# Kernel tuning notes

Measured on AMD Instinct MI355X. Metric: run time of the kernel, lower is better.

## Reference

```python
import jax, jax.numpy as jnp
import numpy as np

ALPHA = 0.2  # leaky_relu negative slope
NFEAT = 3    # node_feat_size for final tanh slice


def _init_linear(key, out_f, in_f):
    kw, kb = jax.random.split(key)
    scale = 1.0 / np.sqrt(in_f)
    w = jax.random.uniform(kw, (out_f, in_f), jnp.float32, -scale, scale)
    b = jax.random.uniform(kb, (out_f,), jnp.float32, -scale, scale)
    return w, b


def setup_inputs() -> dict:
    key = jax.random.key(0)
    ks = jax.random.split(key, 8)
    B, N, H = 64, 100, 32
    inp = {"x": jax.random.normal(ks[0], (B, N, H), jnp.float32)}
    # fe: [65 -> 96 -> 160 -> 192]; fn: [224 -> 256 -> 256 -> 32]
    fe_dims = [(96, 65), (160, 96), (192, 160)]
    fn_dims = [(256, 224), (256, 256), (32, 256)]
    for i, (o, f) in enumerate(fe_dims):
        w, b = _init_linear(ks[1 + i], o, f)
        inp[f"fe_w{i}"] = w
        inp[f"fe_b{i}"] = b
    for i, (o, f) in enumerate(fn_dims):
        w, b = _init_linear(ks[4 + i], o, f)
        inp[f"fn_w{i}"] = w
        inp[f"fn_b{i}"] = b
    return inp


def _forward(x, fe_params, fn_params):
    B, N, H = x.shape
    # --- getA: all-pairs edge features (pos_diffs) ---
    x1 = jnp.broadcast_to(x[:, :, None, :], (B, N, N, H))  # sender i
    x2 = jnp.broadcast_to(x[:, None, :, :], (B, N, N, H))  # receiver j
    dists = jnp.linalg.norm(x2[..., :2] - x1[..., :2] + 1e-12, axis=-1, keepdims=True)
    A = jnp.concatenate([x1, x2, dists], axis=-1)  # [B,N,N,2H+1]
    # --- edge MLP (all layers with leaky_relu) ---
    for w, b in fe_params:
        A = jax.nn.leaky_relu(jnp.einsum("bijf,of->bijo", A, w) + b, ALPHA)
    # sum-aggregate over neighbor axis j
    A = jnp.sum(A, axis=2)  # [B,N,fe_out]
    # --- node MLP (leaky_relu on all but last) ---
    h = jnp.concatenate([A, x], axis=-1)  # [B,N,fe_out+H]
    for w, b in fn_params[:-1]:
        h = jax.nn.leaky_relu(jnp.einsum("bnf,of->bno", h, w) + b, ALPHA)
    w, b = fn_params[-1]
    h = jnp.einsum("bnf,of->bno", h, w) + b  # [B,N,H]
    return jnp.tanh(h[..., :NFEAT])


def reference(x, fe_w0, fe_b0, fe_w1, fe_b1, fe_w2, fe_b2,
              fn_w0, fn_b0, fn_w1, fn_b1, fn_w2, fn_b2):
    fe_params = [(fe_w0, fe_b0), (fe_w1, fe_b1), (fe_w2, fe_b2)]
    fn_params = [(fn_w0, fn_b0), (fn_w1, fn_b1), (fn_w2, fn_b2)]
    return _forward(x, fe_params, fn_params)
```

## Files before the change

kernel.cpp:

```cpp
#include <hip/hip_runtime.h>
#include <math.h>

#define ALPHA 0.2f

typedef __attribute__((ext_vector_type(8))) short bf16x8;
typedef __attribute__((ext_vector_type(4))) float f32x4;

static __device__ __forceinline__ float lrelu(float v) {
    return fmaxf(v, ALPHA * v);
}
static __device__ __forceinline__ uint16_t f2b(float f) {
    union { float f; uint32_t u; } c; c.f = f;
    const uint32_t u = c.u + 0x7FFFu + ((c.u >> 16) & 1u);
    return (uint16_t)(u >> 16);
}
static __device__ __forceinline__ uint32_t cvt2(float lo, float hi) {
    uint32_t r;
    asm("v_cvt_pk_bf16_f32 %0, %1, %2" : "=v"(r) : "v"(lo), "v"(hi));
    return r;
}

__global__ __launch_bounds__(256) void precompute(
    const float* __restrict__ x, const float* __restrict__ w0,
    const float* __restrict__ b0, const float* __restrict__ w1,
    const float* __restrict__ w2, const float* __restrict__ f0,
    const float* __restrict__ f1,
    float* __restrict__ base0T, float* __restrict__ Gp,
    float* __restrict__ xyt, float* __restrict__ wd0,
    uint16_t* __restrict__ wb1, uint16_t* __restrict__ wb2,
    uint16_t* __restrict__ wfn0, uint16_t* __restrict__ wfn1,
    float* __restrict__ hin)
{
    const int blk = blockIdx.x, t = threadIdx.x;
    if (blk >= 256) {
        const int t0 = (blk - 256) * 256 + t;
        for (int i = t0; i < 160 * 96;  i += 7168) wb1[i]  = f2b(w1[i]);
        for (int i = t0; i < 192 * 160; i += 7168) wb2[i]  = f2b(w2[i]);
        for (int i = t0; i < 256 * 224; i += 7168) wfn0[i] = f2b(f0[i]);
        for (int i = t0; i < 256 * 256; i += 7168) wfn1[i] = f2b(f1[i]);
        if (t0 < 96) wd0[t0] = w0[t0 * 65 + 64];
        return;
    }
    __shared__ float W0s[96 * 65];
    __shared__ float xs[25 * 32];
    const int r0 = blk * 25;
    for (int i = t; i < 96 * 65; i += 256) W0s[i] = w0[i];
    for (int i = t; i < 800; i += 256) xs[i] = x[r0 * 32 + i];
    __syncthreads();
    for (int it = 0; it < 19; ++it) {
        const int q = t + 256 * it;
        if (q < 4800) {
            const int row = q / 192, oi = q - row * 192;
            const int o = (oi < 96) ? oi : oi - 96;
            const float* wr = W0s + o * 65 + ((oi < 96) ? 0 : 32);
            const float* xr = xs + row * 32;
            float a = (oi < 96) ? b0[o] : 0.0f;
#pragma unroll
            for (int k = 0; k < 32; ++k) a += wr[k] * xr[k];
            if (oi < 96) base0T[(r0 + row) * 96 + o] = a;
            else         Gp[(o >> 3) * 51200 + (r0 + row) * 8 + (o & 7)] = a;
        }
    }
    for (int i = t; i < 50; i += 256)
        xyt[(r0 + (i >> 1)) * 2 + (i & 1)] = xs[(i >> 1) * 32 + (i & 1)];
    for (int i = t; i < 800; i += 256)
        hin[(r0 + (i >> 5)) * 256 + 192 + (i & 31)] = xs[i];
}

__global__ __launch_bounds__(256, 3) void edge_kernel(
    const float* __restrict__ base0T, const float* __restrict__ Gp,
    const float* __restrict__ xyt, const float* __restrict__ wd0,
    const float* __restrict__ b1f, const float* __restrict__ b2f,
    const uint16_t* __restrict__ wb1, const uint16_t* __restrict__ wb2,
    float* __restrict__ hin, float* __restrict__ PB)
{
    __shared__ __align__(16) uint16_t H1[64 * 104];
    __shared__ __align__(16) uint16_t H2[64 * 168];

    const int bi = blockIdx.x >> 1, half = blockIdx.x & 1, b = bi / 100;
    const int t = threadIdx.x, lane = t & 63, w = t >> 6;
    const int col = lane & 15, g = lane >> 4;
    const int MT = half ? 3 : 4;

    const float2 pi = *(const float2*)(xyt + 2 * bi);

    for (int q = t; q < 768; q += 256) {
        const int row = q & 63, c8 = q >> 6;
        const int jloc = half * 64 + row;
        uint16_t* dst = H1 + row * 104 + c8 * 8;
        if (jloc < 100) {
            const int jg = b * 100 + jloc;
            const float2 pj = *(const float2*)(xyt + 2 * jg);
            const float dx = pj.x - pi.x + 1e-12f, dy = pj.y - pi.y + 1e-12f;
            const float d = sqrtf(dx * dx + dy * dy);
            const int ow = c8 * 8;
            const float* gp = Gp + c8 * 51200 + jg * 8;
            const f32x4 g0 = *(const f32x4*)(gp);
            const f32x4 g1 = *(const f32x4*)(gp + 4);
            const f32x4 c0 = *(const f32x4*)(base0T + bi * 96 + ow);
            const f32x4 c1 = *(const f32x4*)(base0T + bi * 96 + ow + 4);
            const f32x4 w0v = *(const f32x4*)(wd0 + ow);
            const f32x4 w1v = *(const f32x4*)(wd0 + ow + 4);
            float v[8];
#pragma unroll
            for (int e = 0; e < 4; ++e) {
                v[e]     = lrelu(g0[e] + c0[e] + w0v[e] * d);
                v[4 + e] = lrelu(g1[e] + c1[e] + w1v[e] * d);
            }
            *(uint4*)dst = (uint4){cvt2(v[0], v[1]), cvt2(v[2], v[3]),
                                   cvt2(v[4], v[5]), cvt2(v[6], v[7])};
        } else {
            *(uint4*)dst = (uint4){0u, 0u, 0u, 0u};
        }
    }
    __syncthreads();

    {
        f32x4 acc[3][4];
#pragma unroll
        for (int s = 0; s < 3; ++s) {
            const int nt = w + 4 * s;
            if (nt < 10) {
#pragma unroll
                for (int m = 0; m < 4; ++m) if (m < MT) {
                    float bv = b1f[nt * 16 + col];
                    if (half && m == 2 && g != 0) bv = 0.0f;
                    acc[s][m] = (f32x4){bv, bv, bv, bv};
                }
            }
        }
        __builtin_amdgcn_s_setprio(1);
#pragma unroll
        for (int kt = 0; kt < 3; ++kt) {
            bf16x8 bfr[3];
#pragma unroll
            for (int s = 0; s < 3; ++s) {
                const int nt = w + 4 * s;
                if (nt < 10)
                    bfr[s] = *(const bf16x8*)(wb1 + (nt * 16 + col) * 96 + kt * 32 + 8 * g);
            }
#pragma unroll
            for (int m = 0; m < 4; ++m) if (m < MT) {
                const bf16x8 af = *(const bf16x8*)(H1 + (m * 16 + col) * 104 + kt * 32 + 8 * g);
#pragma unroll
                for (int s = 0; s < 3; ++s) {
                    const int nt = w + 4 * s;
                    if (nt < 10)
                        acc[s][m] = __builtin_amdgcn_mfma_f32_16x16x32_bf16(af, bfr[s], acc[s][m], 0, 0, 0);
                }
            }
        }
        __builtin_amdgcn_s_setprio(0);
#pragma unroll
        for (int s = 0; s < 3; ++s) {
            const int nt = w + 4 * s;
            if (nt < 10) {
#pragma unroll
                for (int m = 0; m < 4; ++m) if (m < MT) {
                    const uint32_t p01 = cvt2(lrelu(acc[s][m][0]), lrelu(acc[s][m][1]));
                    const uint32_t p23 = cvt2(lrelu(acc[s][m][2]), lrelu(acc[s][m][3]));
                    const int base = (m * 16 + 4 * g) * 168 + nt * 16 + col;
                    H2[base]       = (uint16_t)p01;
                    H2[base + 168] = (uint16_t)(p01 >> 16);
                    H2[base + 336] = (uint16_t)p23;
                    H2[base + 504] = (uint16_t)(p23 >> 16);
                }
            }
        }
    }
    __syncthreads();

    {
        f32x4 acc[3][4];
#pragma unroll
        for (int s = 0; s < 3; ++s) {
            const int nt = w + 4 * s;
#pragma unroll
            for (int m = 0; m < 4; ++m) if (m < MT) {
                float bv = b2f[nt * 16 + col];
                if (half && m == 2 && g != 0) bv = 0.0f;
                acc[s][m] = (f32x4){bv, bv, bv, bv};
            }
        }
        __builtin_amdgcn_s_setprio(1);
#pragma unroll
        for (int kt = 0; kt < 5; ++kt) {
            bf16x8 bfr[3];
#pragma unroll
            for (int s = 0; s < 3; ++s) {
                const int nt = w + 4 * s;
                bfr[s] = *(const bf16x8*)(wb2 + (nt * 16 + col) * 160 + kt * 32 + 8 * g);
            }
#pragma unroll
            for (int m = 0; m < 4; ++m) if (m < MT) {
                const bf16x8 af = *(const bf16x8*)(H2 + (m * 16 + col) * 168 + kt * 32 + 8 * g);
#pragma unroll
                for (int s = 0; s < 3; ++s)
                    acc[s][m] = __builtin_amdgcn_mfma_f32_16x16x32_bf16(af, bfr[s], acc[s][m], 0, 0, 0);
            }
        }
        __builtin_amdgcn_s_setprio(0);
        float* dst = half ? (PB + bi * 192) : (hin + bi * 256);
#pragma unroll
        for (int s = 0; s < 3; ++s) {
            float ps = 0.0f;
#pragma unroll
            for (int m = 0; m < 4; ++m) if (m < MT) {
#pragma unroll
                for (int r = 0; r < 4; ++r)
                    ps += lrelu(acc[s][m][r]);
            }
            ps += __shfl_xor(ps, 16);
            ps += __shfl_xor(ps, 32);
            if (lane < 16) dst[(w + 4 * s) * 16 + col] = ps;
        }
    }
}

__global__ __launch_bounds__(256) void node_kernel(
    const float* __restrict__ hin, const float* __restrict__ PB,
    const uint16_t* __restrict__ wfn0, const float* __restrict__ fb0,
    const uint16_t* __restrict__ wfn1, const float* __restrict__ fb1,
    const float* __restrict__ fw2, const float* __restrict__ fb2,
    float* __restrict__ out)
{
    __shared__ __align__(16) uint16_t RA[16 * 264];
    __shared__ __align__(16) uint16_t RH[16 * 264];
    const int t = threadIdx.x, lane = t & 63, wave = t >> 6;
    const int col = lane & 15, g = lane >> 4;
    const int r0 = blockIdx.x * 16;

    for (int r = wave; r < 16; r += 4) {
        const float* src = hin + (r0 + r) * 256;
        const float* pbr = PB + (r0 + r) * 192;
        for (int c = lane; c < 224; c += 64) {
            float v = src[c];
            if (c < 192) v += pbr[c];
            RA[r * 232 + c] = f2b(v);
        }
    }
    __syncthreads();
    {
        f32x4 acc[4];
#pragma unroll
        for (int s = 0; s < 4; ++s) {
            const float bv = fb0[(wave + 4 * s) * 16 + col];
            acc[s] = (f32x4){bv, bv, bv, bv};
        }
#pragma unroll
        for (int kt = 0; kt < 7; ++kt) {
            const bf16x8 afr = *(const bf16x8*)(RA + col * 232 + kt * 32 + 8 * g);
#pragma unroll
            for (int s = 0; s < 4; ++s) {
                const bf16x8 bfr = *(const bf16x8*)(
                    wfn0 + ((wave + 4 * s) * 16 + col) * 224 + kt * 32 + 8 * g);
                acc[s] = __builtin_amdgcn_mfma_f32_16x16x32_bf16(afr, bfr, acc[s], 0, 0, 0);
            }
        }
#pragma unroll
        for (int s = 0; s < 4; ++s)
#pragma unroll
            for (int r = 0; r < 4; ++r)
                RH[(4 * g + r) * 264 + (wave + 4 * s) * 16 + col] = f2b(lrelu(acc[s][r]));
    }
    __syncthreads();
    {
        f32x4 acc[4];
#pragma unroll
        for (int s = 0; s < 4; ++s) {
            const float bv = fb1[(wave + 4 * s) * 16 + col];
            acc[s] = (f32x4){bv, bv, bv, bv};
        }
#pragma unroll
        for (int kt = 0; kt < 8; ++kt) {
            const bf16x8 afr = *(const bf16x8*)(RH + col * 264 + kt * 32 + 8 * g);
#pragma unroll
            for (int s = 0; s < 4; ++s) {
                const bf16x8 bfr = *(const bf16x8*)(
                    wfn1 + ((wave + 4 * s) * 16 + col) * 256 + kt * 32 + 8 * g);
                acc[s] = __builtin_amdgcn_mfma_f32_16x16x32_bf16(afr, bfr, acc[s], 0, 0, 0);
            }
        }
        __syncthreads();
#pragma unroll
        for (int s = 0; s < 4; ++s)
#pragma unroll
            for (int r = 0; r < 4; ++r)
                RA[(4 * g + r) * 264 + (wave + 4 * s) * 16 + col] = f2b(lrelu(acc[s][r]));
    }
    __syncthreads();
    const int row = t >> 4, u = t & 15;
    float h = 0.0f;
    if (u < 12) {
        const int o = u >> 2, ks = u & 3;
        const float* wv = fw2 + o * 256 + ks * 64;
        const uint16_t* hr = RA + row * 264 + ks * 64;
        float a = 0.0f;
#pragma unroll 8
        for (int k = 0; k < 64; k += 4) {
            const ushort4 hv = *(const ushort4*)(hr + k);
            union { uint32_t u; float f; } c0, c1, c2, c3;
            c0.u = (uint32_t)hv.x << 16; c1.u = (uint32_t)hv.y << 16;
            c2.u = (uint32_t)hv.z << 16; c3.u = (uint32_t)hv.w << 16;
            a += wv[k] * c0.f + wv[k + 1] * c1.f + wv[k + 2] * c2.f + wv[k + 3] * c3.f;
        }
        h = a;
    }
    h += __shfl_xor(h, 1);
    h += __shfl_xor(h, 2);
    if (u < 12 && (u & 3) == 0)
        out[(r0 + row) * 3 + (u >> 2)] = tanhf(h + fb2[u >> 2]);
}

extern "C" void kernel_launch(void* const* d_in, const int* in_sizes, int n_in,
                              void* d_out, int out_size, void* d_ws, size_t ws_size,
                              hipStream_t stream) {
    (void)in_sizes; (void)n_in; (void)out_size; (void)ws_size;
    const float* x     = (const float*)d_in[0];
    const float* fe_w0 = (const float*)d_in[1];
    const float* fe_b0 = (const float*)d_in[2];
    const float* fe_w1 = (const float*)d_in[3];
    const float* fe_b1 = (const float*)d_in[4];
    const float* fe_w2 = (const float*)d_in[5];
    const float* fe_b2 = (const float*)d_in[6];
    const float* fn_w0 = (const float*)d_in[7];
    const float* fn_b0 = (const float*)d_in[8];
    const float* fn_w1 = (const float*)d_in[9];
    const float* fn_b1 = (const float*)d_in[10];
    const float* fn_w2 = (const float*)d_in[11];
    const float* fn_b2 = (const float*)d_in[12];
    float* out = (float*)d_out;

    float* buf0   = (float*)d_ws;
    float* base0T = buf0 + (size_t)6400 * 256;
    float* Gp     = base0T + 6400 * 96;
    float* xyt    = Gp + 6400 * 96;
    float* wd0    = xyt + 12800;
    uint16_t* wb1  = (uint16_t*)(wd0 + 128);
    uint16_t* wb2  = wb1 + 160 * 96;
    uint16_t* wfn0 = wb2 + 192 * 160;
    uint16_t* wfn1 = wfn0 + 256 * 224;
    float* PB = (float*)(wfn1 + 256 * 256);

    precompute<<<284, 256, 0, stream>>>(x, fe_w0, fe_b0, fe_w1, fe_w2,
                                        fn_w0, fn_w1,
                                        base0T, Gp, xyt, wd0,
                                        wb1, wb2, wfn0, wfn1, buf0);
    edge_kernel<<<12800, 256, 0, stream>>>(base0T, Gp, xyt, wd0,
                                           fe_b1, fe_b2, wb1, wb2, buf0, PB);
    node_kernel<<<400, 256, 0, stream>>>(buf0, PB, wfn0, fn_b0, wfn1, fn_b1,
                                         fn_w2, fn_b2, out);
}
```

Baseline: 163.9 us.

## Transpose layer-1 MFMA output for vector LDS stores and retile layer-2 waves 2x2

Layer-1 MFMA operands are swapped so each lane holds four consecutive output features of one row. That allows a single 8-byte LDS store per tile instead of four scattered 16-bit stores, and a vector bias load. Layer 2 changes from each wave covering all row tiles over 3 column tiles to a 2x2 wave grid: each wave takes 2 row tiles by 6 column tiles, which cuts the weight fragment loads per row tile. The two row-halves' partial sums are then combined through a small shared buffer with an extra barrier. This adds register pressure (12 accumulators plus 6 weight fragments) and one more synchronization.

```diff
diff --git a/kernel.cpp b/kernel.cpp
--- a/kernel.cpp
+++ b/kernel.cpp
@@ -76,6 +76,7 @@
 {
     __shared__ __align__(16) uint16_t H1[64 * 104];
     __shared__ __align__(16) uint16_t H2[64 * 168];
+    __shared__ __align__(16) float part[192];
 
     const int bi = blockIdx.x >> 1, half = blockIdx.x & 1, b = bi / 100;
     const int t = threadIdx.x, lane = t & 63, w = t >> 6;
@@ -121,32 +122,32 @@
         for (int s = 0; s < 3; ++s) {
             const int nt = w + 4 * s;
             if (nt < 10) {
+                const f32x4 bb = *(const f32x4*)(b1f + nt * 16 + 4 * g);
 #pragma unroll
                 for (int m = 0; m < 4; ++m) if (m < MT) {
-                    float bv = b1f[nt * 16 + col];
-                    if (half && m == 2 && g != 0) bv = 0.0f;
-                    acc[s][m] = (f32x4){bv, bv, bv, bv};
+                    const bool pad = (half && m == 2 && col >= 4);
+                    acc[s][m] = pad ? (f32x4){0.f, 0.f, 0.f, 0.f} : bb;
                 }
             }
         }
         __builtin_amdgcn_s_setprio(1);
 #pragma unroll
         for (int kt = 0; kt < 3; ++kt) {
-            bf16x8 bfr[3];
+            bf16x8 wfr[3];
 #pragma unroll
             for (int s = 0; s < 3; ++s) {
                 const int nt = w + 4 * s;
                 if (nt < 10)
-                    bfr[s] = *(const bf16x8*)(wb1 + (nt * 16 + col) * 96 + kt * 32 + 8 * g);
+                    wfr[s] = *(const bf16x8*)(wb1 + (nt * 16 + col) * 96 + kt * 32 + 8 * g);
             }
 #pragma unroll
             for (int m = 0; m < 4; ++m) if (m < MT) {
-                const bf16x8 af = *(const bf16x8*)(H1 + (m * 16 + col) * 104 + kt * 32 + 8 * g);
+                const bf16x8 hf = *(const bf16x8*)(H1 + (m * 16 + col) * 104 + kt * 32 + 8 * g);
 #pragma unroll
                 for (int s = 0; s < 3; ++s) {
                     const int nt = w + 4 * s;
                     if (nt < 10)
-                        acc[s][m] = __builtin_amdgcn_mfma_f32_16x16x32_bf16(af, bfr[s], acc[s][m], 0, 0, 0);
+                        acc[s][m] = __builtin_amdgcn_mfma_f32_16x16x32_bf16(wfr[s], hf, acc[s][m], 0, 0, 0);
                 }
             }
         }
@@ -159,11 +160,8 @@
                 for (int m = 0; m < 4; ++m) if (m < MT) {
                     const uint32_t p01 = cvt2(lrelu(acc[s][m][0]), lrelu(acc[s][m][1]));
                     const uint32_t p23 = cvt2(lrelu(acc[s][m][2]), lrelu(acc[s][m][3]));
-                    const int base = (m * 16 + 4 * g) * 168 + nt * 16 + col;
-                    H2[base]       = (uint16_t)p01;
-                    H2[base + 168] = (uint16_t)(p01 >> 16);
-                    H2[base + 336] = (uint16_t)p23;
-                    H2[base + 504] = (uint16_t)(p23 >> 16);
+                    *(uint2*)(H2 + (m * 16 + col) * 168 + nt * 16 + 4 * g) =
+                        (uint2){p01, p23};
                 }
             }
         }
@@ -171,48 +169,71 @@
     __syncthreads();
 
     {
-        f32x4 acc[3][4];
-#pragma unroll
-        for (int s = 0; s < 3; ++s) {
-            const int nt = w + 4 * s;
-#pragma unroll
-            for (int m = 0; m < 4; ++m) if (m < MT) {
-                float bv = b2f[nt * 16 + col];
-                if (half && m == 2 && g != 0) bv = 0.0f;
-                acc[s][m] = (f32x4){bv, bv, bv, bv};
+        const int wm = w & 1, wn = w >> 1;
+        const int m0 = 2 * wm;
+        f32x4 acc[6][2];
+#pragma unroll
+        for (int s = 0; s < 6; ++s) {
+            const int nt = wn + 2 * s;
+            const float bv = b2f[nt * 16 + col];
+#pragma unroll
+            for (int u = 0; u < 2; ++u) {
+                const int m = m0 + u;
+                if (half && m == 3) continue;
+                float bvm = bv;
+                if (half && m == 2 && g != 0) bvm = 0.0f;
+                acc[s][u] = (f32x4){bvm, bvm, bvm, bvm};
             }
         }
         __builtin_amdgcn_s_setprio(1);
 #pragma unroll
         for (int kt = 0; kt < 5; ++kt) {
-            bf16x8 bfr[3];
-#pragma unroll
-            for (int s = 0; s < 3; ++s) {
-                const int nt = w + 4 * s;
-                bfr[s] = *(const bf16x8*)(wb2 + (nt * 16 + col) * 160 + kt * 32 + 8 * g);
-            }
-#pragma unroll
-            for (int m = 0; m < 4; ++m) if (m < MT) {
+            bf16x8 wfr[6];
+#pragma unroll
+            for (int s = 0; s < 6; ++s) {
+                const int nt = wn + 2 * s;
+                wfr[s] = *(const bf16x8*)(wb2 + (nt * 16 + col) * 160 + kt * 32 + 8 * g);
+            }
+#pragma unroll
+            for (int u = 0; u < 2; ++u) {
+                const int m = m0 + u;
+                if (half && m == 3) continue;
                 const bf16x8 af = *(const bf16x8*)(H2 + (m * 16 + col) * 168 + kt * 32 + 8 * g);
 #pragma unroll
-                for (int s = 0; s < 3; ++s)
-                    acc[s][m] = __builtin_amdgcn_mfma_f32_16x16x32_bf16(af, bfr[s], acc[s][m], 0, 0, 0);
+                for (int s = 0; s < 6; ++s)
+                    acc[s][u] = __builtin_amdgcn_mfma_f32_16x16x32_bf16(af, wfr[s], acc[s][u], 0, 0, 0);
             }
         }
         __builtin_amdgcn_s_setprio(0);
-        float* dst = half ? (PB + bi * 192) : (hin + bi * 256);
-#pragma unroll
-        for (int s = 0; s < 3; ++s) {
-            float ps = 0.0f;
-#pragma unroll
-            for (int m = 0; m < 4; ++m) if (m < MT) {
+        float ps[6];
+#pragma unroll
+        for (int s = 0; s < 6; ++s) {
+            float p = 0.0f;
+#pragma unroll
+            for (int u = 0; u < 2; ++u) {
+                const int m = m0 + u;
+                if (half && m == 3) continue;
 #pragma unroll
                 for (int r = 0; r < 4; ++r)
-                    ps += lrelu(acc[s][m][r]);
-            }
-            ps += __shfl_xor(ps, 16);
-            ps += __shfl_xor(ps, 32);
-            if (lane < 16) dst[(w + 4 * s) * 16 + col] = ps;
+                    p += lrelu(acc[s][u][r]);
+            }
+            p += __shfl_xor(p, 16);
+            p += __shfl_xor(p, 32);
+            ps[s] = p;
+        }
+        if (wm == 0 && lane < 16) {
+#pragma unroll
+            for (int s = 0; s < 6; ++s)
+                part[(wn + 2 * s) * 16 + col] = ps[s];
+        }
+        __syncthreads();
+        if (wm == 1 && lane < 16) {
+            float* dst = half ? (PB + bi * 192) : (hin + bi * 256);
+#pragma unroll
+            for (int s = 0; s < 6; ++s) {
+                const int nt = wn + 2 * s;
+                dst[nt * 16 + col] = ps[s] + part[nt * 16 + col];
+            }
         }
     }
 }
```

After: 206.0 us. 1.26x slower.
